# Optimization experiments

Measured on AMD Instinct MI355X. Metric: run time of the kernel, lower is better.

Reference implementation:

```python
import jax, jax.numpy as jnp
import numpy as np


def setup_inputs() -> dict:
    key = jax.random.key(0)
    k_x, k_we, k_wd = jax.random.split(key, 3)
    N, D, L, K = 4096, 2048, 32768, 32
    x = jax.random.normal(k_x, (N, D), dtype=jnp.float32)
    # Encoder: nn.Linear(d_in, num_latents) -> weight [L, D], bias zeroed in __init__
    W_enc = jax.random.normal(k_we, (L, D), dtype=jnp.float32) * (1.0 / np.sqrt(D))
    b_enc = jnp.zeros((L,), dtype=jnp.float32)
    # Decoder: W_dec initialized as encoder clone then unit-normalized per latent row
    W_dec = jax.random.normal(k_wd, (L, D), dtype=jnp.float32)
    W_dec = W_dec / (jnp.linalg.norm(W_dec, axis=1, keepdims=True) + 1e-7)
    b_dec = jnp.zeros((D,), dtype=jnp.float32)
    return {"x": x, "W_enc": W_enc, "b_enc": b_enc, "W_dec": W_dec, "b_dec": b_dec, "k": K}


def reference(x, W_enc, b_enc, W_dec, b_dec, k):
    # sae_in = x - b_dec (non-transcode path)
    sae_in = x - b_dec                                   # [N, D]
    # pre_acts = relu(encoder(sae_in))
    pre_acts = jax.nn.relu(sae_in @ W_enc.T + b_enc)     # [N, L]
    # select_topk (activation == 'topk')
    top_acts, top_idx = jax.lax.top_k(pre_acts, k)       # [N, k]
    # decoder_impl: gather active decoder rows and weighted-sum into output
    sae_out = jnp.einsum('nk,nkd->nd', top_acts, W_dec[top_idx]) + b_dec  # [N, D]
    # FVU (y = x, dead_mask=None, multi_topk=False)
    e = x - sae_out
    total_variance = jnp.sum((x - jnp.mean(x, axis=0)) ** 2)
    fvu = jnp.sum(e ** 2) / total_variance
    auxk_loss = jnp.zeros((), dtype=sae_out.dtype)
    multi_topk_fvu = jnp.zeros((), dtype=sae_out.dtype)
    return sae_out, top_acts, top_idx, fvu, auxk_loss, multi_topk_fvu
```

## Files before the change

kernel.cpp:

```cpp
#include <hip/hip_runtime.h>
#include <hip/hip_bf16.h>

#define NR 4096
#define DIMD 2048
#define NL 32768
#define KTOP 32
#define CAP 224
#define THRQ 2.80f

typedef float f32x4 __attribute__((ext_vector_type(4)));
typedef __bf16 bf16x8 __attribute__((ext_vector_type(8)));

__device__ inline unsigned short f2bf(float f) {
  union { float fl; unsigned u; } v; v.fl = f;
  unsigned u = v.u;
  u = (u + 0x7fffu + ((u >> 16) & 1u)) >> 16;
  return (unsigned short)u;
}

__device__ __forceinline__ void gload_lds16(const void* g, void* l) {
  __builtin_amdgcn_global_load_lds(
      (const __attribute__((address_space(1))) unsigned int*)g,
      (__attribute__((address_space(3))) unsigned int*)l, 16, 0, 0);
}

__global__ __launch_bounds__(256) void k_rowstats(const float* __restrict__ x,
    const float* __restrict__ bdec, unsigned short* __restrict__ xb,
    float* __restrict__ thr, double* __restrict__ sumx2) {
  int row = blockIdx.x, tid = threadIdx.x;
  const float4* xr = (const float4*)(x + (size_t)row * DIMD);
  const float4* bd = (const float4*)bdec;
  ushort4* xbr = (ushort4*)(xb + (size_t)row * DIMD);
  float sx = 0.f, si = 0.f;
  for (int i = tid; i < DIMD / 4; i += 256) {
    float4 v = xr[i]; float4 b = bd[i];
    sx += v.x * v.x + v.y * v.y + v.z * v.z + v.w * v.w;
    float a0 = v.x - b.x, a1 = v.y - b.y, a2 = v.z - b.z, a3 = v.w - b.w;
    si += a0 * a0 + a1 * a1 + a2 * a2 + a3 * a3;
    ushort4 o; o.x = f2bf(a0); o.y = f2bf(a1); o.z = f2bf(a2); o.w = f2bf(a3);
    xbr[i] = o;
  }
  __shared__ double r1[256], r2[256];
  r1[tid] = (double)sx; r2[tid] = (double)si; __syncthreads();
  for (int o = 128; o > 0; o >>= 1) {
    if (tid < o) { r1[tid] += r1[tid + o]; r2[tid] += r2[tid + o]; }
    __syncthreads();
  }
  if (tid == 0) {
    thr[row] = THRQ * sqrtf((float)(r2[0] / (double)DIMD));
    atomicAdd(sumx2, r1[0]);
  }
}

__global__ __launch_bounds__(256) void k_colsum(const float* __restrict__ x,
                                                double* __restrict__ colsum) {
  int col = blockIdx.x * 256 + threadIdx.x;
  int r0 = blockIdx.y * 64;
  double s = 0.0;
  for (int r = 0; r < 64; r++) s += (double)x[(size_t)(r0 + r) * DIMD + col];
  atomicAdd(&colsum[col], s);
}

__global__ __launch_bounds__(256) void k_convw(const float* __restrict__ w,
                                               unsigned short* __restrict__ wb) {
  size_t total = (size_t)NL * DIMD / 8;
  for (size_t i = (size_t)blockIdx.x * 256 + threadIdx.x; i < total;
       i += (size_t)gridDim.x * 256) {
    float4 a = ((const float4*)w)[2 * i], b = ((const float4*)w)[2 * i + 1];
    ushort4 o1, o2;
    o1.x = f2bf(a.x); o1.y = f2bf(a.y); o1.z = f2bf(a.z); o1.w = f2bf(a.w);
    o2.x = f2bf(b.x); o2.y = f2bf(b.y); o2.z = f2bf(b.z); o2.w = f2bf(b.w);
    ((ushort4*)wb)[2 * i] = o1; ((ushort4*)wb)[2 * i + 1] = o2;
  }
}

__global__ __launch_bounds__(512, 2) void k_gemm3(const unsigned short* __restrict__ xb,
    const unsigned short* __restrict__ wb, const float* __restrict__ benc,
    const float* __restrict__ thr, int* __restrict__ cnt, int* __restrict__ cand,
    float* __restrict__ candv) {
  __shared__ __align__(16) char lds[131072];
  int tid = threadIdx.x;
  int wv = tid >> 6, lane = tid & 63;
  int wm = wv >> 2, wn = wv & 3;
  int lq = lane >> 4, lr = lane & 15;
  int bid = blockIdx.x;
  int xcd = bid & 7, chunk = bid >> 3;
  int ntile = xcd * 16 + (chunk >> 4);
  int mtile = chunk & 15;
  const unsigned short* Ag = xb + (size_t)(mtile * 256) * DIMD;
  const unsigned short* Bg = wb + (size_t)(ntile * 256) * DIMD;

  f32x4 acc[8][4];
#pragma unroll
  for (int m = 0; m < 8; m++)
#pragma unroll
    for (int n = 0; n < 4; n++) { acc[m][n][0] = 0.f; acc[m][n][1] = 0.f; acc[m][n][2] = 0.f; acc[m][n][3] = 0.f; }

  int ra0 = tid >> 3;
  int sa0 = ((tid & 7) ^ (ra0 & 7)) * 8;
#define STAGEU(gb, r0, loff) { \
    gload_lds16((gb) + (size_t)((r0) + ra0) * DIMD + sa0, lds + (loff) + tid * 16); \
    gload_lds16((gb) + (size_t)((r0) + ra0 + 64) * DIMD + sa0, lds + (loff) + tid * 16 + 8192); }

  int s0 = (lq ^ (lr & 7)) << 4;

#define WAITV(N) { asm volatile("s_waitcnt vmcnt(" #N ")" ::: "memory"); \
                   __builtin_amdgcn_sched_barrier(0); }

#define MFMA16(mb, A0, A1, A2, A3, B0, B1, B2, B3) { \
    __builtin_amdgcn_s_setprio(1); \
    acc[(mb)+0][0] = __builtin_amdgcn_mfma_f32_16x16x32_bf16(A0, B0, acc[(mb)+0][0], 0, 0, 0); \
    acc[(mb)+1][0] = __builtin_amdgcn_mfma_f32_16x16x32_bf16(A1, B0, acc[(mb)+1][0], 0, 0, 0); \
    acc[(mb)+2][0] = __builtin_amdgcn_mfma_f32_16x16x32_bf16(A2, B0, acc[(mb)+2][0], 0, 0, 0); \
    acc[(mb)+3][0] = __builtin_amdgcn_mfma_f32_16x16x32_bf16(A3, B0, acc[(mb)+3][0], 0, 0, 0); \
    acc[(mb)+0][1] = __builtin_amdgcn_mfma_f32_16x16x32_bf16(A0, B1, acc[(mb)+0][1], 0, 0, 0); \
    acc[(mb)+1][1] = __builtin_amdgcn_mfma_f32_16x16x32_bf16(A1, B1, acc[(mb)+1][1], 0, 0, 0); \
    acc[(mb)+2][1] = __builtin_amdgcn_mfma_f32_16x16x32_bf16(A2, B1, acc[(mb)+2][1], 0, 0, 0); \
    acc[(mb)+3][1] = __builtin_amdgcn_mfma_f32_16x16x32_bf16(A3, B1, acc[(mb)+3][1], 0, 0, 0); \
    acc[(mb)+0][2] = __builtin_amdgcn_mfma_f32_16x16x32_bf16(A0, B2, acc[(mb)+0][2], 0, 0, 0); \
    acc[(mb)+1][2] = __builtin_amdgcn_mfma_f32_16x16x32_bf16(A1, B2, acc[(mb)+1][2], 0, 0, 0); \
    acc[(mb)+2][2] = __builtin_amdgcn_mfma_f32_16x16x32_bf16(A2, B2, acc[(mb)+2][2], 0, 0, 0); \
    acc[(mb)+3][2] = __builtin_amdgcn_mfma_f32_16x16x32_bf16(A3, B2, acc[(mb)+3][2], 0, 0, 0); \
    acc[(mb)+0][3] = __builtin_amdgcn_mfma_f32_16x16x32_bf16(A0, B3, acc[(mb)+0][3], 0, 0, 0); \
    acc[(mb)+1][3] = __builtin_amdgcn_mfma_f32_16x16x32_bf16(A1, B3, acc[(mb)+1][3], 0, 0, 0); \
    acc[(mb)+2][3] = __builtin_amdgcn_mfma_f32_16x16x32_bf16(A2, B3, acc[(mb)+2][3], 0, 0, 0); \
    acc[(mb)+3][3] = __builtin_amdgcn_mfma_f32_16x16x32_bf16(A3, B3, acc[(mb)+3][3], 0, 0, 0); \
    __builtin_amdgcn_s_setprio(0); }

  STAGEU(Ag, 0, 0);
  STAGEU(Bg, 0, 65536);
  STAGEU(Bg, 128, 65536 + 16384);
  STAGEU(Ag, 128, 16384);

  for (int kt = 0; kt < 32; kt++) {
    int cur = kt & 1, nxt = cur ^ 1;
    bool pre = (kt < 31);
    const unsigned short* Agn = Ag + (kt + 1) * 64;
    const unsigned short* Bgn = Bg + (kt + 1) * 64;
    const char* Ac = lds + cur * 32768;
    const char* Bc = lds + 65536 + cur * 32768;
    WAITV(2);
    __builtin_amdgcn_s_barrier();
    if (pre) STAGEU(Agn, 0, nxt * 32768);
    bf16x8 b0 = *(const bf16x8*)(Bc + (0 * 64 + wn * 16 + lr) * 128 + s0);
    bf16x8 b1 = *(const bf16x8*)(Bc + (1 * 64 + wn * 16 + lr) * 128 + s0);
    bf16x8 b2 = *(const bf16x8*)(Bc + (2 * 64 + wn * 16 + lr) * 128 + s0);
    bf16x8 b3 = *(const bf16x8*)(Bc + (3 * 64 + wn * 16 + lr) * 128 + s0);
    {
      bf16x8 a0 = *(const bf16x8*)(Ac + (0 * 32 + wm * 16 + lr) * 128 + s0);
      bf16x8 a1 = *(const bf16x8*)(Ac + (1 * 32 + wm * 16 + lr) * 128 + s0);
      bf16x8 a2 = *(const bf16x8*)(Ac + (2 * 32 + wm * 16 + lr) * 128 + s0);
      bf16x8 a3 = *(const bf16x8*)(Ac + (3 * 32 + wm * 16 + lr) * 128 + s0);
      MFMA16(0, a0, a1, a2, a3, b0, b1, b2, b3);
    }
    if (pre) { WAITV(2); } else { WAITV(0); }
    __builtin_amdgcn_s_barrier();
    if (pre) STAGEU(Bgn, 0, 65536 + nxt * 32768);
    {
      bf16x8 a0 = *(const bf16x8*)(Ac + (4 * 32 + wm * 16 + lr) * 128 + s0);
      bf16x8 a1 = *(const bf16x8*)(Ac + (5 * 32 + wm * 16 + lr) * 128 + s0);
      bf16x8 a2 = *(const bf16x8*)(Ac + (6 * 32 + wm * 16 + lr) * 128 + s0);
      bf16x8 a3 = *(const bf16x8*)(Ac + (7 * 32 + wm * 16 + lr) * 128 + s0);
      MFMA16(4, a0, a1, a2, a3, b0, b1, b2, b3);
    }
    if (pre) STAGEU(Bgn, 128, 65536 + nxt * 32768 + 16384);
    b0 = *(const bf16x8*)(Bc + (0 * 64 + wn * 16 + lr) * 128 + (s0 ^ 64));
    b1 = *(const bf16x8*)(Bc + (1 * 64 + wn * 16 + lr) * 128 + (s0 ^ 64));
    b2 = *(const bf16x8*)(Bc + (2 * 64 + wn * 16 + lr) * 128 + (s0 ^ 64));
    b3 = *(const bf16x8*)(Bc + (3 * 64 + wn * 16 + lr) * 128 + (s0 ^ 64));
    {
      bf16x8 a0 = *(const bf16x8*)(Ac + (0 * 32 + wm * 16 + lr) * 128 + (s0 ^ 64));
      bf16x8 a1 = *(const bf16x8*)(Ac + (1 * 32 + wm * 16 + lr) * 128 + (s0 ^ 64));
      bf16x8 a2 = *(const bf16x8*)(Ac + (2 * 32 + wm * 16 + lr) * 128 + (s0 ^ 64));
      bf16x8 a3 = *(const bf16x8*)(Ac + (3 * 32 + wm * 16 + lr) * 128 + (s0 ^ 64));
      MFMA16(0, a0, a1, a2, a3, b0, b1, b2, b3);
    }
    if (pre) STAGEU(Agn, 128, nxt * 32768 + 16384);
    {
      bf16x8 a0 = *(const bf16x8*)(Ac + (4 * 32 + wm * 16 + lr) * 128 + (s0 ^ 64));
      bf16x8 a1 = *(const bf16x8*)(Ac + (5 * 32 + wm * 16 + lr) * 128 + (s0 ^ 64));
      bf16x8 a2 = *(const bf16x8*)(Ac + (6 * 32 + wm * 16 + lr) * 128 + (s0 ^ 64));
      bf16x8 a3 = *(const bf16x8*)(Ac + (7 * 32 + wm * 16 + lr) * 128 + (s0 ^ 64));
      MFMA16(4, a0, a1, a2, a3, b0, b1, b2, b3);
    }
  }
#undef STAGEU
#undef WAITV
#undef MFMA16
#pragma unroll
  for (int m = 0; m < 8; m++) {
    int rbase = mtile * 256 + m * 32 + wm * 16 + lq * 4;
#pragma unroll
    for (int j = 0; j < 4; j++) {
      int grow = rbase + j;
      float tv = thr[grow];
#pragma unroll
      for (int n = 0; n < 4; n++) {
        int gcol = ntile * 256 + n * 64 + wn * 16 + lr;
        float v = acc[m][n][j] + benc[gcol];
        if (v > tv) {
          int p = atomicAdd(&cnt[grow], 1);
          if (p < CAP) { cand[grow * CAP + p] = gcol; candv[grow * CAP + p] = v; }
        }
      }
    }
  }
}

__global__ __launch_bounds__(256) void k_refine_saeout(const float* __restrict__ x,
    const float* __restrict__ bdec, const float* __restrict__ w,
    const float* __restrict__ benc, const int* __restrict__ cnt,
    const int* __restrict__ cand, const float* __restrict__ candv,
    const float* __restrict__ thr, const float* __restrict__ wdec,
    float* __restrict__ out, double* __restrict__ sume2) {
  int row = blockIdx.x, tid = threadIdx.x;
  __shared__ float xs[DIMD];
  __shared__ float sv[256]; __shared__ int sl[256];
  __shared__ float sa[KTOP]; __shared__ int si[KTOP];
  __shared__ float a32s;
  __shared__ double red[256];
  const float* xr = x + (size_t)row * DIMD;
  for (int i = tid; i < DIMD; i += 256) xs[i] = xr[i] - bdec[i];
  int c = min(cnt[row], CAP);
  float mya = -3.0e38f; int mylat = 0x7fffffff;
  if (tid < c) { mya = candv[row * CAP + tid]; mylat = cand[row * CAP + tid]; }
  sv[tid] = mya;
  if (tid == 0) a32s = -3.0e38f;
  __syncthreads();
  if (tid < c) {
    int r = 0;
    for (int j = 0; j < c; j++) {
      float vj = sv[j];
      r += (vj > mya) || (vj == mya && j < tid);
    }
    if (r == KTOP - 1) a32s = mya;
  }
  __syncthreads();
  float cutoff = a32s - 0.008f * thr[row];
  float myv = -3.0e38f;
  if (tid < c && mya >= cutoff) {
    const float* wr = w + (size_t)mylat * DIMD;
    const int pb[5] = {0, 512, 1024, 1536, 2048};
    float accv = 0.f;
#pragma unroll
    for (int p = 0; p < 4; p++) {
      float s = 0.f;
      for (int k = pb[p]; k < pb[p + 1]; k += 4) {
        float4 wv = *(const float4*)(wr + k);
        s = fmaf(xs[k],     wv.x, s);
        s = fmaf(xs[k + 1], wv.y, s);
        s = fmaf(xs[k + 2], wv.z, s);
        s = fmaf(xs[k + 3], wv.w, s);
      }
      accv += s;
    }
    myv = accv + benc[mylat];
  }
  sv[tid] = myv; sl[tid] = (myv > -2.9e38f) ? mylat : 0x7fffffff;
  if (tid < KTOP) { sa[tid] = 0.f; si[tid] = 0; }
  __syncthreads();
  if (myv > -2.9e38f) {
    int rk = 0;
    for (int j = 0; j < c; j++) {
      float vj = sv[j]; int lj = sl[j];
      rk += (vj > myv) || (vj == myv && lj < mylat);
    }
    if (rk < KTOP) { sa[rk] = myv; si[rk] = mylat; }
  }
  __syncthreads();
  if (tid < KTOP) {
    out[(size_t)NR * DIMD + row * KTOP + tid] = sa[tid];
    out[(size_t)NR * DIMD + (size_t)NR * KTOP + row * KTOP + tid] = (float)si[tid];
  }
  int c0 = tid * 4, c1 = 1024 + tid * 4;
  float a00 = 0, a01 = 0, a02 = 0, a03 = 0, a10 = 0, a11 = 0, a12 = 0, a13 = 0;
  for (int k = 0; k < KTOP; k++) {
    const float* wr = wdec + (size_t)si[k] * DIMD;
    float av = sa[k];
    float4 w0 = *(const float4*)(wr + c0);
    float4 w1 = *(const float4*)(wr + c1);
    a00 += av * w0.x; a01 += av * w0.y; a02 += av * w0.z; a03 += av * w0.w;
    a10 += av * w1.x; a11 += av * w1.y; a12 += av * w1.z; a13 += av * w1.w;
  }
  float4 b0 = *(const float4*)(bdec + c0), b1 = *(const float4*)(bdec + c1);
  a00 += b0.x; a01 += b0.y; a02 += b0.z; a03 += b0.w;
  a10 += b1.x; a11 += b1.y; a12 += b1.z; a13 += b1.w;
  float4 x0 = *(const float4*)(xr + c0), x1 = *(const float4*)(xr + c1);
  float4 o0, o1;
  o0.x = a00; o0.y = a01; o0.z = a02; o0.w = a03;
  o1.x = a10; o1.y = a11; o1.z = a12; o1.w = a13;
  *(float4*)(out + (size_t)row * DIMD + c0) = o0;
  *(float4*)(out + (size_t)row * DIMD + c1) = o1;
  double es = 0.0; float e;
  e = x0.x - a00; es += (double)e * e; e = x0.y - a01; es += (double)e * e;
  e = x0.z - a02; es += (double)e * e; e = x0.w - a03; es += (double)e * e;
  e = x1.x - a10; es += (double)e * e; e = x1.y - a11; es += (double)e * e;
  e = x1.z - a12; es += (double)e * e; e = x1.w - a13; es += (double)e * e;
  red[tid] = es; __syncthreads();
  for (int o = 128; o > 0; o >>= 1) { if (tid < o) red[tid] += red[tid + o]; __syncthreads(); }
  if (tid == 0) atomicAdd(sume2, red[0]);
}

__global__ __launch_bounds__(256) void k_final(const double* __restrict__ colsum,
    const double* __restrict__ sumx2, const double* __restrict__ sume2,
    float* __restrict__ out) {
  int tid = threadIdx.x;
  double s = 0.0;
  for (int i = tid; i < DIMD; i += 256) { double v = colsum[i]; s += v * v; }
  __shared__ double red[256];
  red[tid] = s; __syncthreads();
  for (int o = 128; o > 0; o >>= 1) { if (tid < o) red[tid] += red[tid + o]; __syncthreads(); }
  if (tid == 0) {
    double tv = *sumx2 - red[0] / (double)NR;
    double fvu = *sume2 / tv;
    size_t base = (size_t)NR * DIMD + 2 * (size_t)NR * KTOP;
    out[base] = (float)fvu;
    out[base + 1] = 0.f;
    out[base + 2] = 0.f;
  }
}

extern "C" void kernel_launch(void* const* d_in, const int* in_sizes, int n_in,
                              void* d_out, int out_size, void* d_ws, size_t ws_size,
                              hipStream_t stream) {
  const float* x    = (const float*)d_in[0];
  const float* wenc = (const float*)d_in[1];
  const float* benc = (const float*)d_in[2];
  const float* wdec = (const float*)d_in[3];
  const float* bdec = (const float*)d_in[4];
  float* out = (float*)d_out;
  char* ws = (char*)d_ws;

  unsigned short* xb  = (unsigned short*)(ws + 0);
  float* thr          = (float*)(ws + 16777216);
  int* cnt            = (int*)(ws + 16793600);
  int* cand           = (int*)(ws + 16809984);
  double* colsum      = (double*)(ws + 21528576);
  double* sumx2       = (double*)(ws + 21544960);
  double* sume2       = sumx2 + 1;
  unsigned short* wb  = (unsigned short*)(ws + 22020096);
  float* candv        = (float*)(ws + 156237824);

  hipMemsetAsync(cnt, 0, 4096 * 4, stream);
  hipMemsetAsync(colsum, 0, 2048 * 8 + 16, stream);

  k_rowstats<<<NR, 256, 0, stream>>>(x, bdec, xb, thr, sumx2);
  k_colsum<<<dim3(8, 64), 256, 0, stream>>>(x, colsum);
  k_convw<<<2048, 256, 0, stream>>>(wenc, wb);
  k_gemm3<<<2048, 512, 0, stream>>>(xb, wb, benc, thr, cnt, cand, candv);
  k_refine_saeout<<<NR, 256, 0, stream>>>(x, bdec, wenc, benc, cnt, cand, candv, thr, wdec, out, sume2);
  k_final<<<1, 256, 0, stream>>>(colsum, sumx2, sume2, out);
}
```

Measured before the change: 1.054 ms.

## Halve GEMM K-tile to 32 so LDS fits two blocks per CU

```diff
diff --git a/kernel.cpp b/kernel.cpp
--- a/kernel.cpp
+++ b/kernel.cpp
@@ -74,11 +74,11 @@
   }
 }
 
-__global__ __launch_bounds__(512, 2) void k_gemm3(const unsigned short* __restrict__ xb,
+__global__ __launch_bounds__(512, 2) void k_gemm5(const unsigned short* __restrict__ xb,
     const unsigned short* __restrict__ wb, const float* __restrict__ benc,
     const float* __restrict__ thr, int* __restrict__ cnt, int* __restrict__ cand,
     float* __restrict__ candv) {
-  __shared__ __align__(16) char lds[131072];
+  __shared__ __align__(16) char lds[65536];
   int tid = threadIdx.x;
   int wv = tid >> 6, lane = tid & 63;
   int wm = wv >> 2, wn = wv & 3;
@@ -96,16 +96,22 @@
 #pragma unroll
     for (int n = 0; n < 4; n++) { acc[m][n][0] = 0.f; acc[m][n][1] = 0.f; acc[m][n][2] = 0.f; acc[m][n][3] = 0.f; }
 
-  int ra0 = tid >> 3;
-  int sa0 = ((tid & 7) ^ (ra0 & 7)) * 8;
-#define STAGEU(gb, r0, loff) { \
-    gload_lds16((gb) + (size_t)((r0) + ra0) * DIMD + sa0, lds + (loff) + tid * 16); \
-    gload_lds16((gb) + (size_t)((r0) + ra0 + 64) * DIMD + sa0, lds + (loff) + tid * 16 + 8192); }
-
-  int s0 = (lq ^ (lr & 7)) << 4;
-
-#define WAITV(N) { asm volatile("s_waitcnt vmcnt(" #N ")" ::: "memory"); \
-                   __builtin_amdgcn_sched_barrier(0); }
+  int c0 = tid, c1 = tid + 512;
+  int r0c = c0 >> 2, r1c = c1 >> 2;
+  size_t gsrc0 = (size_t)r0c * DIMD + (size_t)(((c0 & 3) ^ ((r0c >> 1) & 3)) * 8);
+  size_t gsrc1 = (size_t)r1c * DIMD + (size_t)(((c1 & 3) ^ ((r1c >> 1) & 3)) * 8);
+  int d0 = c0 * 16, d1 = c1 * 16;
+#define STAGEU(gb, loff) { \
+    gload_lds16((gb) + gsrc0, lds + (loff) + d0); \
+    gload_lds16((gb) + gsrc1, lds + (loff) + d1); }
+
+  int fA = ((wm * 8) + (lr >> 1)) & 3;
+  int fB = ((wn * 8) + (lr >> 1)) & 3;
+  int colA = (lq ^ fA) << 4;
+  int colB = (lq ^ fB) << 4;
+
+#define WAITV0 { asm volatile("s_waitcnt vmcnt(0)" ::: "memory"); \
+                 __builtin_amdgcn_sched_barrier(0); }
 
 #define MFMA16(mb, A0, A1, A2, A3, B0, B1, B2, B3) { \
     __builtin_amdgcn_s_setprio(1); \
@@ -127,65 +133,41 @@
     acc[(mb)+3][3] = __builtin_amdgcn_mfma_f32_16x16x32_bf16(A3, B3, acc[(mb)+3][3], 0, 0, 0); \
     __builtin_amdgcn_s_setprio(0); }
 
-  STAGEU(Ag, 0, 0);
-  STAGEU(Bg, 0, 65536);
-  STAGEU(Bg, 128, 65536 + 16384);
-  STAGEU(Ag, 128, 16384);
-
-  for (int kt = 0; kt < 32; kt++) {
+  STAGEU(Ag, 0);
+  STAGEU(Bg, 32768);
+
+  for (int kt = 0; kt < 64; kt++) {
     int cur = kt & 1, nxt = cur ^ 1;
-    bool pre = (kt < 31);
-    const unsigned short* Agn = Ag + (kt + 1) * 64;
-    const unsigned short* Bgn = Bg + (kt + 1) * 64;
-    const char* Ac = lds + cur * 32768;
-    const char* Bc = lds + 65536 + cur * 32768;
-    WAITV(2);
+    bool pre = (kt < 63);
+    const unsigned short* Agn = Ag + (kt + 1) * 32;
+    const unsigned short* Bgn = Bg + (kt + 1) * 32;
+    const char* Ac = lds + cur * 16384;
+    const char* Bc = lds + 32768 + cur * 16384;
+    WAITV0;
     __builtin_amdgcn_s_barrier();
-    if (pre) STAGEU(Agn, 0, nxt * 32768);
-    bf16x8 b0 = *(const bf16x8*)(Bc + (0 * 64 + wn * 16 + lr) * 128 + s0);
-    bf16x8 b1 = *(const bf16x8*)(Bc + (1 * 64 + wn * 16 + lr) * 128 + s0);
-    bf16x8 b2 = *(const bf16x8*)(Bc + (2 * 64 + wn * 16 + lr) * 128 + s0);
-    bf16x8 b3 = *(const bf16x8*)(Bc + (3 * 64 + wn * 16 + lr) * 128 + s0);
+    if (pre) STAGEU(Agn, nxt * 16384);
+    bf16x8 b0 = *(const bf16x8*)(Bc + (0 * 64 + wn * 16 + lr) * 64 + colB);
+    bf16x8 b1 = *(const bf16x8*)(Bc + (1 * 64 + wn * 16 + lr) * 64 + colB);
+    bf16x8 b2 = *(const bf16x8*)(Bc + (2 * 64 + wn * 16 + lr) * 64 + colB);
+    bf16x8 b3 = *(const bf16x8*)(Bc + (3 * 64 + wn * 16 + lr) * 64 + colB);
     {
-      bf16x8 a0 = *(const bf16x8*)(Ac + (0 * 32 + wm * 16 + lr) * 128 + s0);
-      bf16x8 a1 = *(const bf16x8*)(Ac + (1 * 32 + wm * 16 + lr) * 128 + s0);
-      bf16x8 a2 = *(const bf16x8*)(Ac + (2 * 32 + wm * 16 + lr) * 128 + s0);
-      bf16x8 a3 = *(const bf16x8*)(Ac + (3 * 32 + wm * 16 + lr) * 128 + s0);
+      bf16x8 a0 = *(const bf16x8*)(Ac + (0 * 32 + wm * 16 + lr) * 64 + colA);
+      bf16x8 a1 = *(const bf16x8*)(Ac + (1 * 32 + wm * 16 + lr) * 64 + colA);
+      bf16x8 a2 = *(const bf16x8*)(Ac + (2 * 32 + wm * 16 + lr) * 64 + colA);
+      bf16x8 a3 = *(const bf16x8*)(Ac + (3 * 32 + wm * 16 + lr) * 64 + colA);
       MFMA16(0, a0, a1, a2, a3, b0, b1, b2, b3);
     }
-    if (pre) { WAITV(2); } else { WAITV(0); }
-    __builtin_amdgcn_s_barrier();
-    if (pre) STAGEU(Bgn, 0, 65536 + nxt * 32768);
+    if (pre) STAGEU(Bgn, 32768 + nxt * 16384);
     {
-      bf16x8 a0 = *(const bf16x8*)(Ac + (4 * 32 + wm * 16 + lr) * 128 + s0);
-      bf16x8 a1 = *(const bf16x8*)(Ac + (5 * 32 + wm * 16 + lr) * 128 + s0);
-      bf16x8 a2 = *(const bf16x8*)(Ac + (6 * 32 + wm * 16 + lr) * 128 + s0);
-      bf16x8 a3 = *(const bf16x8*)(Ac + (7 * 32 + wm * 16 + lr) * 128 + s0);
+      bf16x8 a0 = *(const bf16x8*)(Ac + (4 * 32 + wm * 16 + lr) * 64 + colA);
+      bf16x8 a1 = *(const bf16x8*)(Ac + (5 * 32 + wm * 16 + lr) * 64 + colA);
+      bf16x8 a2 = *(const bf16x8*)(Ac + (6 * 32 + wm * 16 + lr) * 64 + colA);
+      bf16x8 a3 = *(const bf16x8*)(Ac + (7 * 32 + wm * 16 + lr) * 64 + colA);
       MFMA16(4, a0, a1, a2, a3, b0, b1, b2, b3);
     }
-    if (pre) STAGEU(Bgn, 128, 65536 + nxt * 32768 + 16384);
-    b0 = *(const bf16x8*)(Bc + (0 * 64 + wn * 16 + lr) * 128 + (s0 ^ 64));
-    b1 = *(const bf16x8*)(Bc + (1 * 64 + wn * 16 + lr) * 128 + (s0 ^ 64));
-    b2 = *(const bf16x8*)(Bc + (2 * 64 + wn * 16 + lr) * 128 + (s0 ^ 64));
-    b3 = *(const bf16x8*)(Bc + (3 * 64 + wn * 16 + lr) * 128 + (s0 ^ 64));
-    {
-      bf16x8 a0 = *(const bf16x8*)(Ac + (0 * 32 + wm * 16 + lr) * 128 + (s0 ^ 64));
-      bf16x8 a1 = *(const bf16x8*)(Ac + (1 * 32 + wm * 16 + lr) * 128 + (s0 ^ 64));
-      bf16x8 a2 = *(const bf16x8*)(Ac + (2 * 32 + wm * 16 + lr) * 128 + (s0 ^ 64));
-      bf16x8 a3 = *(const bf16x8*)(Ac + (3 * 32 + wm * 16 + lr) * 128 + (s0 ^ 64));
-      MFMA16(0, a0, a1, a2, a3, b0, b1, b2, b3);
-    }
-    if (pre) STAGEU(Agn, 128, nxt * 32768 + 16384);
-    {
-      bf16x8 a0 = *(const bf16x8*)(Ac + (4 * 32 + wm * 16 + lr) * 128 + (s0 ^ 64));
-      bf16x8 a1 = *(const bf16x8*)(Ac + (5 * 32 + wm * 16 + lr) * 128 + (s0 ^ 64));
-      bf16x8 a2 = *(const bf16x8*)(Ac + (6 * 32 + wm * 16 + lr) * 128 + (s0 ^ 64));
-      bf16x8 a3 = *(const bf16x8*)(Ac + (7 * 32 + wm * 16 + lr) * 128 + (s0 ^ 64));
-      MFMA16(4, a0, a1, a2, a3, b0, b1, b2, b3);
-    }
   }
 #undef STAGEU
-#undef WAITV
+#undef WAITV0
 #undef MFMA16
 #pragma unroll
   for (int m = 0; m < 8; m++) {
@@ -347,7 +329,7 @@
   k_rowstats<<<NR, 256, 0, stream>>>(x, bdec, xb, thr, sumx2);
   k_colsum<<<dim3(8, 64), 256, 0, stream>>>(x, colsum);
   k_convw<<<2048, 256, 0, stream>>>(wenc, wb);
-  k_gemm3<<<2048, 512, 0, stream>>>(xb, wb, benc, thr, cnt, cand, candv);
+  k_gemm5<<<2048, 512, 0, stream>>>(xb, wb, benc, thr, cnt, cand, candv);
   k_refine_saeout<<<NR, 256, 0, stream>>>(x, bdec, wenc, benc, cnt, cand, candv, thr, wdec, out, sume2);
   k_final<<<1, 256, 0, stream>>>(colsum, sumx2, sume2, out);
 }
```

After: 1.150 ms. 1.09x slower.
